# Optimization experiments

Hardware: AMD Instinct MI355X
Metric: run time of the kernel (lower is better)

The kernel has to match this reference:

```python
import jax, jax.numpy as jnp
import numpy as np

N_NODES = 50000
N_EDGES = 800000
D_IN = 128
D_HID = 128
D_OUT = 128
N_GRAPHS = 512


def _linear_params(key, d_in, d_out):
    kw, kb = jax.random.split(key)
    bound = 1.0 / np.sqrt(d_in)
    W = jax.random.uniform(kw, (d_in, d_out), minval=-bound, maxval=bound, dtype=jnp.float32)
    b = jax.random.uniform(kb, (d_out,), minval=-bound, maxval=bound, dtype=jnp.float32)
    return W, b


def setup_inputs() -> dict:
    key = jax.random.key(0)
    ks = jax.random.split(key, 8)
    x = jax.random.normal(ks[0], (N_NODES, D_IN), dtype=jnp.float32)
    edge_index = jax.random.randint(ks[1], (2, N_EDGES), 0, N_NODES, dtype=jnp.int64)
    batch = jnp.sort(jax.random.randint(ks[2], (N_NODES,), 0, N_GRAPHS, dtype=jnp.int64))
    W1a, b1a = _linear_params(ks[3], D_IN, D_HID)
    W1b, b1b = _linear_params(ks[4], D_HID, D_HID)
    W2a, b2a = _linear_params(ks[5], D_HID, D_HID)
    W2b, b2b = _linear_params(ks[6], D_HID, D_OUT)
    Wfc, bfc = _linear_params(ks[7], D_OUT, D_OUT)
    return {"x": x, "edge_index": edge_index, "batch": batch,
            "W1a": W1a, "b1a": b1a, "W1b": W1b, "b1b": b1b,
            "W2a": W2a, "b2a": b2a, "W2b": W2b, "b2b": b2b,
            "Wfc": Wfc, "bfc": bfc}


def _gin_conv(h, src, dst, Wa, ba, Wb, bb):
    # neighbor sum: gather source features, scatter-add to targets (eps=0)
    agg = jax.ops.segment_sum(h[src], dst, num_segments=N_NODES)
    z = h + agg  # (1+eps)*x + sum_neighbors, eps=0
    z = jax.nn.relu(z @ Wa + ba)
    return z @ Wb + bb


def reference(x, edge_index, batch, W1a, b1a, W1b, b1b, W2a, b2a, W2b, b2b, Wfc, bfc):
    src, dst = edge_index[0], edge_index[1]
    h = jax.nn.relu(_gin_conv(x, src, dst, W1a, b1a, W1b, b1b))
    h = jax.nn.relu(_gin_conv(h, src, dst, W2a, b2a, W2b, b2b))
    g = jax.ops.segment_sum(h, batch, num_segments=N_GRAPHS)  # global_add_pool
    return jax.nn.relu(g @ Wfc + bfc)
```

## Files before the change

### kernel.cpp

```cpp
#include <hip/hip_runtime.h>

#define N_NODES 50000
#define N_EDGES 800000
#define N_GRAPHS 512
#define CAP 48
#define ZN N_NODES

typedef __bf16 bf16x8 __attribute__((ext_vector_type(8)));
typedef float f32x4 __attribute__((ext_vector_type(4)));
typedef unsigned short u16;
typedef unsigned int u32;

__device__ __forceinline__ u16 f2bf(float f) {
    union { float f; u32 i; } v; v.f = f;
    u32 r = v.i + 0x7fffu + ((v.i >> 16) & 1u);
    return (u16)(r >> 16);
}
__device__ __forceinline__ float bf2f(u16 u) {
    union { u32 i; float f; } v; v.i = ((u32)u) << 16; return v.f;
}

__global__ void k_prep(const int* __restrict__ ei, int* __restrict__ cnt, u16* __restrict__ slots,
                       const float* __restrict__ X, u16* __restrict__ XB, u16* __restrict__ HB,
                       const float* __restrict__ W1a, const float* __restrict__ W1b,
                       const float* __restrict__ W2a, const float* __restrict__ W2b,
                       u16* __restrict__ T1a, u16* __restrict__ T1b,
                       u16* __restrict__ T2a, u16* __restrict__ T2b,
                       int E, int n4) {
    int bid = blockIdx.x;
    if (bid < 3125) {
        int e = bid * 256 + threadIdx.x;
        if (e < E) {
            int s = ei[e];
            int d = ei[E + e];
            int p = atomicAdd(&cnt[d * 4], 1);
            if (p < CAP) slots[(size_t)d * CAP + p] = (u16)s;
        }
    } else if (bid < 9375) {
        int i = (bid - 3125) * 256 + threadIdx.x;
        if (i < n4) {
            float4 v = ((const float4*)X)[i];
            ushort4 o;
            o.x = f2bf(v.x); o.y = f2bf(v.y); o.z = f2bf(v.z); o.w = f2bf(v.w);
            ((ushort4*)XB)[i] = o;
        }
    } else if (bid < 9631) {
        int b2 = bid - 9375;
        int widx = b2 >> 6;
        int i = (b2 & 63) * 256 + threadIdx.x;
        const float* W = widx == 0 ? W1a : widx == 1 ? W1b : widx == 2 ? W2a : W2b;
        u16* T = widx == 0 ? T1a : widx == 1 ? T1b : widx == 2 ? T2a : T2b;
        int k = i >> 7, n = i & 127;
        T[n * 128 + k] = f2bf(W[k * 128 + n]);
    } else {
        int t = threadIdx.x;
        if (t < 64)       ((u32*)XB)[(size_t)ZN * 64 + t]        = 0u;
        else if (t < 128) ((u32*)HB)[(size_t)ZN * 64 + (t - 64)] = 0u;
    }
}


#define STAGE16(BUF, CI, CJ)                                            \
    _Pragma("unroll")                                                   \
    for (int u = 0; u < 16; ++u) {                                      \
        u32 nb = (u32)smI[wv][(CI)][(CJ) + u];                          \
        BUF[u] = X2[(nb << 6) + lane];                                  \
    }

#define ACCUM16(BUF)                                                    \
    _Pragma("unroll")                                                   \
    for (int u = 0; u < 16; ++u) {                                      \
        ax += bf2f((u16)(BUF[u] & 0xffff));                             \
        ay += bf2f((u16)(BUF[u] >> 16));                                \
    }

#define FINROW(CI) {                                                    \
        int r = wv * 8 + (CI);                                          \
        smZu[(r * 16 + ((lane >> 2) ^ (r & 15))) * 4 + (lane & 3)] =    \
            (((u32)f2bf(ay)) << 16) | (u32)f2bf(ax);                    \
        ax = 0.f; ay = 0.f;                                             \
    }

#define AGG_PHASE()                                                                  \
    int degv = 0;                                                                    \
    {                                                                                \
        int gr = row0 + wv * 8 + lane;                                               \
        if (lane < 8 && gr < N) {                                                    \
            int d = cnt[gr * 4];                                                     \
            degv = d > CAP ? CAP : d;                                                \
        }                                                                            \
    }                                                                                \
    {                                                                                \
        u32 tv[8];                                                                   \
        int sl = lane - 1; sl = sl < 0 ? 0 : (sl >= CAP ? CAP - 1 : sl);             \
        _Pragma("unroll")                                                            \
        for (int i = 0; i < 8; ++i) {                                                \
            int gr = row0 + wv * 8 + i;                                              \
            tv[i] = (gr < N) ? (u32)slots[(size_t)gr * CAP + sl] : (u32)ZN;          \
        }                                                                            \
        _Pragma("unroll")                                                            \
        for (int i = 0; i < 8; ++i) {                                                \
            int gr = row0 + wv * 8 + i;                                              \
            int de = __builtin_amdgcn_readlane(degv, i) + 1;                         \
            u32 v = (lane == 0) ? (u32)gr : tv[i];                                   \
            if (gr >= N || lane >= de) v = ZN;                                       \
            smI[wv][i][lane] = (u16)v;                                               \
        }                                                                            \
    }                                                                                \
    {                                                                                \
        float ax = 0.f, ay = 0.f;                                                    \
        u32 bufA[16], bufB[16];                                                      \
        int ci = 0, cj = 0;                                                          \
        int de = __builtin_amdgcn_readlane(degv, 0) + 1;                             \
        STAGE16(bufA, 0, 0);                                                         \
        for (;;) {                                                                   \
            int ni = ci, nj = cj + 16;                                               \
            if (nj >= de) { ni = ci + 1; nj = 0; }                                   \
            int have = (ni < 8);                                                     \
            if (have) { de = __builtin_amdgcn_readlane(degv, ni) + 1;                \
                        STAGE16(bufB, ni, nj); }                                     \
            ACCUM16(bufA);                                                           \
            if (nj == 0) FINROW(ci);                                                 \
            if (!have) break;                                                        \
            ci = ni; cj = nj;                                                        \
            ni = ci; nj = cj + 16;                                                   \
            if (nj >= de) { ni = ci + 1; nj = 0; }                                   \
            have = (ni < 8);                                                         \
            if (have) { de = __builtin_amdgcn_readlane(degv, ni) + 1;                \
                        STAGE16(bufA, ni, nj); }                                     \
            ACCUM16(bufB);                                                           \
            if (nj == 0) FINROW(ci);                                                 \
            if (!have) break;                                                        \
            ci = ni; cj = nj;                                                        \
        }                                                                            \
    }

__global__ __launch_bounds__(512, 4)
void k_gin1(const u16* __restrict__ X, const int* __restrict__ cnt,
            const u16* __restrict__ slots,
            const u16* __restrict__ WaT, const float* __restrict__ ba,
            const u16* __restrict__ WbT, const float* __restrict__ bb,
            u16* __restrict__ H, int N) {
    __shared__ u16 smZ[64 * 128];
    __shared__ u16 smW[128 * 128];
    __shared__ u16 smI[8][8][64];
    uint4* smZ4 = (uint4*)smZ;
    uint4* smW4 = (uint4*)smW;
    u32* smZu = (u32*)smZ;

    const int tid = threadIdx.x;
    const int lane = tid & 63, wv = tid >> 6;
    const int q = lane >> 4, m = lane & 15;
    const int ws = wv & 3, wc = wv >> 2;
    const int row0 = blockIdx.x * 64;
    const u32* X2 = (const u32*)X;

    for (int i = tid; i < 2048; i += 512) {
        int r = i >> 4, c4 = i & 15;
        smW4[r * 16 + (c4 ^ (r & 15))] = ((const uint4*)WaT)[i];
    }

    AGG_PHASE();
    __syncthreads();

    f32x4 acc[4];
#pragma unroll
    for (int nt = 0; nt < 4; ++nt) acc[nt] = (f32x4){0.f, 0.f, 0.f, 0.f};
#pragma unroll
    for (int kt = 0; kt < 4; ++kt) {
        int r = ws * 16 + m;
        bf16x8 a = *(const bf16x8*)(smZ4 + (r * 16 + ((kt * 4 + q) ^ (r & 15))));
#pragma unroll
        for (int nt = 0; nt < 4; ++nt) {
            int n = (wc * 4 + nt) * 16 + m;
            bf16x8 bfr = *(const bf16x8*)(smW4 + (n * 16 + ((kt * 4 + q) ^ (n & 15))));
            acc[nt] = __builtin_amdgcn_mfma_f32_16x16x32_bf16(a, bfr, acc[nt], 0, 0, 0);
        }
    }
    __syncthreads();

    for (int i = tid; i < 2048; i += 512) {
        int r = i >> 4, c4 = i & 15;
        smW4[r * 16 + (c4 ^ (r & 15))] = ((const uint4*)WbT)[i];
    }
#pragma unroll
    for (int nt = 0; nt < 4; ++nt) {
        int col = (wc * 4 + nt) * 16 + m;
        float bias = ba[col];
        int c4 = col >> 3, ci8 = col & 7;
#pragma unroll
        for (int r2 = 0; r2 < 4; ++r2) {
            int row = ws * 16 + q * 4 + r2;
            float x = acc[nt][r2] + bias;
            x = x > 0.f ? x : 0.f;
            smZ[(row * 16 + (c4 ^ (row & 15))) * 8 + ci8] = f2bf(x);
        }
    }
    __syncthreads();

    f32x4 acc2[4];
#pragma unroll
    for (int nt = 0; nt < 4; ++nt) acc2[nt] = (f32x4){0.f, 0.f, 0.f, 0.f};
#pragma unroll
    for (int kt = 0; kt < 4; ++kt) {
        int r = ws * 16 + m;
        bf16x8 a = *(const bf16x8*)(smZ4 + (r * 16 + ((kt * 4 + q) ^ (r & 15))));
#pragma unroll
        for (int nt = 0; nt < 4; ++nt) {
            int n = (wc * 4 + nt) * 16 + m;
            bf16x8 bfr = *(const bf16x8*)(smW4 + (n * 16 + ((kt * 4 + q) ^ (n & 15))));
            acc2[nt] = __builtin_amdgcn_mfma_f32_16x16x32_bf16(a, bfr, acc2[nt], 0, 0, 0);
        }
    }
#pragma unroll
    for (int nt = 0; nt < 4; ++nt) {
        int col = (wc * 4 + nt) * 16 + m;
        float bias = bb[col];
#pragma unroll
        for (int r2 = 0; r2 < 4; ++r2) {
            int row = row0 + ws * 16 + q * 4 + r2;
            if (row < N) {
                float x = acc2[nt][r2] + bias;
                H[(size_t)row * 128 + col] = f2bf(x > 0.f ? x : 0.f);
            }
        }
    }
}

__global__ __launch_bounds__(512, 4)
void k_gin2(const u16* __restrict__ X, const int* __restrict__ cnt,
            const u16* __restrict__ slots,
            const u16* __restrict__ WaT, const float* __restrict__ ba,
            const u16* __restrict__ WbT, const float* __restrict__ bb,
            const int* __restrict__ batch, float* __restrict__ G, int N) {
    __shared__ u16 smZ[64 * 128];
    __shared__ u16 smW[128 * 128];
    __shared__ u16 smI[8][8][64];
    __shared__ int sb[64];
    uint4* smZ4 = (uint4*)smZ;
    uint4* smW4 = (uint4*)smW;
    u32* smZu = (u32*)smZ;

    const int tid = threadIdx.x;
    const int lane = tid & 63, wv = tid >> 6;
    const int q = lane >> 4, m = lane & 15;
    const int ws = wv & 3, wc = wv >> 2;
    const int row0 = blockIdx.x * 64;
    const u32* X2 = (const u32*)X;

    if (tid < 64) sb[tid] = (row0 + tid < N) ? batch[row0 + tid] : -1;

    for (int i = tid; i < 2048; i += 512) {
        int r = i >> 4, c4 = i & 15;
        smW4[r * 16 + (c4 ^ (r & 15))] = ((const uint4*)WaT)[i];
    }

    AGG_PHASE();
    __syncthreads();

    f32x4 acc[4];
#pragma unroll
    for (int nt = 0; nt < 4; ++nt) acc[nt] = (f32x4){0.f, 0.f, 0.f, 0.f};
#pragma unroll
    for (int kt = 0; kt < 4; ++kt) {
        int r = ws * 16 + m;
        bf16x8 a = *(const bf16x8*)(smZ4 + (r * 16 + ((kt * 4 + q) ^ (r & 15))));
#pragma unroll
        for (int nt = 0; nt < 4; ++nt) {
            int n = (wc * 4 + nt) * 16 + m;
            bf16x8 bfr = *(const bf16x8*)(smW4 + (n * 16 + ((kt * 4 + q) ^ (n & 15))));
            acc[nt] = __builtin_amdgcn_mfma_f32_16x16x32_bf16(a, bfr, acc[nt], 0, 0, 0);
        }
    }
    __syncthreads();

    for (int i = tid; i < 2048; i += 512) {
        int r = i >> 4, c4 = i & 15;
        smW4[r * 16 + (c4 ^ (r & 15))] = ((const uint4*)WbT)[i];
    }
#pragma unroll
    for (int nt = 0; nt < 4; ++nt) {
        int col = (wc * 4 + nt) * 16 + m;
        float bias = ba[col];
        int c4 = col >> 3, ci8 = col & 7;
#pragma unroll
        for (int r2 = 0; r2 < 4; ++r2) {
            int row = ws * 16 + q * 4 + r2;
            float x = acc[nt][r2] + bias;
            x = x > 0.f ? x : 0.f;
            smZ[(row * 16 + (c4 ^ (row & 15))) * 8 + ci8] = f2bf(x);
        }
    }
    __syncthreads();

    f32x4 acc2[4];
#pragma unroll
    for (int nt = 0; nt < 4; ++nt) acc2[nt] = (f32x4){0.f, 0.f, 0.f, 0.f};
#pragma unroll
    for (int kt = 0; kt < 4; ++kt) {
        int r = ws * 16 + m;
        bf16x8 a = *(const bf16x8*)(smZ4 + (r * 16 + ((kt * 4 + q) ^ (r & 15))));
#pragma unroll
        for (int nt = 0; nt < 4; ++nt) {
            int n = (wc * 4 + nt) * 16 + m;
            bf16x8 bfr = *(const bf16x8*)(smW4 + (n * 16 + ((kt * 4 + q) ^ (n & 15))));
            acc2[nt] = __builtin_amdgcn_mfma_f32_16x16x32_bf16(a, bfr, acc2[nt], 0, 0, 0);
        }
    }
#pragma unroll
    for (int nt = 0; nt < 4; ++nt) {
        int col = (wc * 4 + nt) * 16 + m;
        float bias = bb[col];
#pragma unroll
        for (int r2 = 0; r2 < 4; ++r2) {
            int row = ws * 16 + q * 4 + r2;
            float x = acc2[nt][r2] + bias;
            smZ[row * 128 + col] = f2bf(x > 0.f ? x : 0.f);
        }
    }
    __syncthreads();
    {
        int col = tid & 127, quarter = tid >> 7;
        int rbeg = quarter * 16, rend = rbeg + 16;
        float run = 0.f; int curg = -1;
        for (int r = rbeg; r < rend; ++r) {
            int gg = sb[r];
            if (gg < 0) break;
            if (gg != curg) {
                if (curg >= 0) atomicAdd(&G[curg * 128 + col], run);
                run = 0.f; curg = gg;
            }
            run += bf2f(smZ[r * 128 + col]);
        }
        if (curg >= 0) atomicAdd(&G[curg * 128 + col], run);
    }
}

__global__ void k_fc(const float* __restrict__ G, const float* __restrict__ W,
                     const float* __restrict__ bias, float* __restrict__ O) {
    __shared__ float gs[128];
    int t = threadIdx.x, gidx = blockIdx.x;
    gs[t] = G[gidx * 128 + t];
    __syncthreads();
    float acc = bias[t];
    for (int k = 0; k < 128; ++k)
        acc += gs[k] * W[k * 128 + t];
    acc = acc > 0.f ? acc : 0.f;
    O[gidx * 128 + t] = acc;
}

extern "C" void kernel_launch(void* const* d_in, const int* in_sizes, int n_in,
                              void* d_out, int out_size, void* d_ws, size_t ws_size,
                              hipStream_t stream) {
    const int N = N_NODES, E = N_EDGES, NG = N_GRAPHS;

    const float* x   = (const float*)d_in[0];
    const int* ei    = (const int*)d_in[1];
    const int* batch = (const int*)d_in[2];
    const float* W1a = (const float*)d_in[3];
    const float* b1a = (const float*)d_in[4];
    const float* W1b = (const float*)d_in[5];
    const float* b1b = (const float*)d_in[6];
    const float* W2a = (const float*)d_in[7];
    const float* b2a = (const float*)d_in[8];
    const float* W2b = (const float*)d_in[9];
    const float* b2b = (const float*)d_in[10];
    const float* Wfc = (const float*)d_in[11];
    const float* bfc = (const float*)d_in[12];
    float* out = (float*)d_out;

    char* w = (char*)d_ws;
    int* cnt    = (int*)(w + 0x0000000);
    float* g    = (float*)(w + 0x00C4000);
    u16* slots  = (u16*)(w + 0x0110000);
    u16* xb     = (u16*)(w + 0x05B0000);
    u16* hb     = (u16*)(w + 0x1F50000);
    u16* T1a    = (u16*)(w + 0x2C20000);
    u16* T1b    = (u16*)(w + 0x2C28000);
    u16* T2a    = (u16*)(w + 0x2C30000);
    u16* T2b    = (u16*)(w + 0x2C38000);

    (void)hipMemsetAsync(w, 0, 0x104000, stream);

    const int n4 = N * 128 / 4;
    k_prep<<<9632, 256, 0, stream>>>(ei, cnt, slots, x, xb, hb, W1a, W1b, W2a, W2b,
                                     T1a, T1b, T2a, T2b, E, n4);

    const int GINB = (N + 63) / 64;

    k_gin1<<<GINB, 512, 0, stream>>>(xb, cnt, slots, T1a, b1a, T1b, b1b, hb, N);
    k_gin2<<<GINB, 512, 0, stream>>>(hb, cnt, slots, T2a, b2a, T2b, b2b, batch, g, N);

    k_fc<<<NG, 128, 0, stream>>>(g, Wfc, bfc, out);
}
```

Baseline: 229.9 us.

## Bin edges per 64-node block and build neighbor lists in shared memory

Edge scatter now does one global atomic per 64-node destination block and appends packed (local dst, src) words into per-block bins, instead of one atomic per destination node into per-node slot arrays. Each GIN kernel reads its block's bin coalesced and builds per-row neighbor lists in LDS with shared atomics, with capacity raised to 64 per row. This is meant to cut contention and scattered global writes in the prep kernel and make the gather-index loads contiguous. In exchange it adds LDS atomics and an extra barrier inside both GIN kernels, and edges are dropped if a bin overflows its 1536 capacity.

```diff
diff --git a/kernel.cpp b/kernel.cpp
--- a/kernel.cpp
+++ b/kernel.cpp
@@ -3,8 +3,9 @@
 #define N_NODES 50000
 #define N_EDGES 800000
 #define N_GRAPHS 512
-#define CAP 48
 #define ZN N_NODES
+#define BCAP 1536
+#define RCAP 64
 
 typedef __bf16 bf16x8 __attribute__((ext_vector_type(8)));
 typedef float f32x4 __attribute__((ext_vector_type(4)));
@@ -20,7 +21,7 @@
     union { u32 i; float f; } v; v.i = ((u32)u) << 16; return v.f;
 }
 
-__global__ void k_prep(const int* __restrict__ ei, int* __restrict__ cnt, u16* __restrict__ slots,
+__global__ void k_prep(const int* __restrict__ ei, int* __restrict__ cur, u32* __restrict__ bins,
                        const float* __restrict__ X, u16* __restrict__ XB, u16* __restrict__ HB,
                        const float* __restrict__ W1a, const float* __restrict__ W1b,
                        const float* __restrict__ W2a, const float* __restrict__ W2b,
@@ -33,8 +34,9 @@
         if (e < E) {
             int s = ei[e];
             int d = ei[E + e];
-            int p = atomicAdd(&cnt[d * 4], 1);
-            if (p < CAP) slots[(size_t)d * CAP + p] = (u16)s;
+            int b = d >> 6;
+            int p = atomicAdd(&cur[b * 32], 1);
+            if (p < BCAP) bins[(size_t)b * BCAP + p] = (((u32)(d & 63)) << 16) | (u32)s;
         }
     } else if (bid < 9375) {
         int i = (bid - 3125) * 256 + threadIdx.x;
@@ -63,7 +65,7 @@
 #define STAGE16(BUF, CI, CJ)                                            \
     _Pragma("unroll")                                                   \
     for (int u = 0; u < 16; ++u) {                                      \
-        u32 nb = (u32)smI[wv][(CI)][(CJ) + u];                          \
+        u32 nb = (u32)smI[wv * 8 + (CI)][(CJ) + u];                     \
         BUF[u] = X2[(nb << 6) + lane];                                  \
     }
 
@@ -82,42 +84,46 @@
     }
 
 #define AGG_PHASE()                                                                  \
-    int degv = 0;                                                                    \
     {                                                                                \
-        int gr = row0 + wv * 8 + lane;                                               \
-        if (lane < 8 && gr < N) {                                                    \
-            int d = cnt[gr * 4];                                                     \
-            degv = d > CAP ? CAP : d;                                                \
+        const u32 fill = 0xC350C350u;                      \
+        int r = tid >> 3, c = tid & 7;                                               \
+        uint4 v4 = make_uint4(fill, fill, fill, fill);                               \
+        if (c == 0) {                                                                \
+            int gr = row0 + r;                                                       \
+            v4.x = (fill & 0xffff0000u) | (u32)((gr < N) ? gr : ZN);                 \
+        }                                                                            \
+        ((uint4*)smI)[tid] = v4;                                                     \
+        if (tid < 64) ldsCnt[tid] = 1;                                               \
+    }                                                                                \
+    __syncthreads();                                                                 \
+    {                                                                                \
+        int ecnt = cur[blockIdx.x * 32];                                             \
+        if (ecnt > BCAP) ecnt = BCAP;                                                \
+        const u32* myb = bins + (size_t)blockIdx.x * BCAP;                           \
+        for (int i = tid; i < ecnt; i += 512) {                                      \
+            u32 v = myb[i];                                                          \
+            int dl = v >> 16;                                                        \
+            int pos = atomicAdd(&ldsCnt[dl], 1);                                     \
+            if (pos < RCAP) smI[dl][pos] = (u16)(v & 0xffff);                        \
         }                                                                            \
     }                                                                                \
-    {                                                                                \
-        u32 tv[8];                                                                   \
-        int sl = lane - 1; sl = sl < 0 ? 0 : (sl >= CAP ? CAP - 1 : sl);             \
-        _Pragma("unroll")                                                            \
-        for (int i = 0; i < 8; ++i) {                                                \
-            int gr = row0 + wv * 8 + i;                                              \
-            tv[i] = (gr < N) ? (u32)slots[(size_t)gr * CAP + sl] : (u32)ZN;          \
-        }                                                                            \
-        _Pragma("unroll")                                                            \
-        for (int i = 0; i < 8; ++i) {                                                \
-            int gr = row0 + wv * 8 + i;                                              \
-            int de = __builtin_amdgcn_readlane(degv, i) + 1;                         \
-            u32 v = (lane == 0) ? (u32)gr : tv[i];                                   \
-            if (gr >= N || lane >= de) v = ZN;                                       \
-            smI[wv][i][lane] = (u16)v;                                               \
-        }                                                                            \
+    __syncthreads();                                                                 \
+    int degv = 0;                                                                    \
+    if (lane < 8) {                                                                  \
+        int d = ldsCnt[wv * 8 + lane];                                               \
+        degv = d > RCAP ? RCAP : d;                                                  \
     }                                                                                \
     {                                                                                \
         float ax = 0.f, ay = 0.f;                                                    \
         u32 bufA[16], bufB[16];                                                      \
         int ci = 0, cj = 0;                                                          \
-        int de = __builtin_amdgcn_readlane(degv, 0) + 1;                             \
+        int de = __builtin_amdgcn_readlane(degv, 0);                                 \
         STAGE16(bufA, 0, 0);                                                         \
         for (;;) {                                                                   \
             int ni = ci, nj = cj + 16;                                               \
             if (nj >= de) { ni = ci + 1; nj = 0; }                                   \
             int have = (ni < 8);                                                     \
-            if (have) { de = __builtin_amdgcn_readlane(degv, ni) + 1;                \
+            if (have) { de = __builtin_amdgcn_readlane(degv, ni);                    \
                         STAGE16(bufB, ni, nj); }                                     \
             ACCUM16(bufA);                                                           \
             if (nj == 0) FINROW(ci);                                                 \
@@ -126,7 +132,7 @@
             ni = ci; nj = cj + 16;                                                   \
             if (nj >= de) { ni = ci + 1; nj = 0; }                                   \
             have = (ni < 8);                                                         \
-            if (have) { de = __builtin_amdgcn_readlane(degv, ni) + 1;                \
+            if (have) { de = __builtin_amdgcn_readlane(degv, ni);                    \
                         STAGE16(bufA, ni, nj); }                                     \
             ACCUM16(bufB);                                                           \
             if (nj == 0) FINROW(ci);                                                 \
@@ -136,14 +142,15 @@
     }
 
 __global__ __launch_bounds__(512, 4)
-void k_gin1(const u16* __restrict__ X, const int* __restrict__ cnt,
-            const u16* __restrict__ slots,
+void k_gin1(const u16* __restrict__ X, const int* __restrict__ cur,
+            const u32* __restrict__ bins,
             const u16* __restrict__ WaT, const float* __restrict__ ba,
             const u16* __restrict__ WbT, const float* __restrict__ bb,
             u16* __restrict__ H, int N) {
     __shared__ u16 smZ[64 * 128];
     __shared__ u16 smW[128 * 128];
-    __shared__ u16 smI[8][8][64];
+    __shared__ u16 smI[64][RCAP];
+    __shared__ int ldsCnt[64];
     uint4* smZ4 = (uint4*)smZ;
     uint4* smW4 = (uint4*)smW;
     u32* smZu = (u32*)smZ;
@@ -228,14 +235,15 @@
 }
 
 __global__ __launch_bounds__(512, 4)
-void k_gin2(const u16* __restrict__ X, const int* __restrict__ cnt,
-            const u16* __restrict__ slots,
+void k_gin2(const u16* __restrict__ X, const int* __restrict__ cur,
+            const u32* __restrict__ bins,
             const u16* __restrict__ WaT, const float* __restrict__ ba,
             const u16* __restrict__ WbT, const float* __restrict__ bb,
             const int* __restrict__ batch, float* __restrict__ G, int N) {
     __shared__ u16 smZ[64 * 128];
     __shared__ u16 smW[128 * 128];
-    __shared__ u16 smI[8][8][64];
+    __shared__ u16 smI[64][RCAP];
+    __shared__ int ldsCnt[64];
     __shared__ int sb[64];
     uint4* smZ4 = (uint4*)smZ;
     uint4* smW4 = (uint4*)smW;
@@ -248,7 +256,10 @@
     const int row0 = blockIdx.x * 64;
     const u32* X2 = (const u32*)X;
 
-    if (tid < 64) sb[tid] = (row0 + tid < N) ? batch[row0 + tid] : -1;
+    if (tid >= 448 && tid < 512) {
+        int t = tid - 448;
+        sb[t] = (row0 + t < N) ? batch[row0 + t] : -1;
+    }
 
     for (int i = tid; i < 2048; i += 512) {
         int r = i >> 4, c4 = i & 15;
@@ -370,26 +381,26 @@
     float* out = (float*)d_out;
 
     char* w = (char*)d_ws;
-    int* cnt    = (int*)(w + 0x0000000);
-    float* g    = (float*)(w + 0x00C4000);
-    u16* slots  = (u16*)(w + 0x0110000);
-    u16* xb     = (u16*)(w + 0x05B0000);
-    u16* hb     = (u16*)(w + 0x1F50000);
-    u16* T1a    = (u16*)(w + 0x2C20000);
-    u16* T1b    = (u16*)(w + 0x2C28000);
-    u16* T2a    = (u16*)(w + 0x2C30000);
-    u16* T2b    = (u16*)(w + 0x2C38000);
-
-    (void)hipMemsetAsync(w, 0, 0x104000, stream);
+    int* cur    = (int*)(w + 0x0000000);
+    float* g    = (float*)(w + 0x0019000);
+    u32* bins   = (u32*)(w + 0x0060000);
+    u16* xb     = (u16*)(w + 0x0500000);
+    u16* hb     = (u16*)(w + 0x1200000);
+    u16* T1a    = (u16*)(w + 0x1F00000);
+    u16* T1b    = (u16*)(w + 0x1F08000);
+    u16* T2a    = (u16*)(w + 0x1F10000);
+    u16* T2b    = (u16*)(w + 0x1F18000);
+
+    (void)hipMemsetAsync(w, 0, 0x59000, stream);
 
     const int n4 = N * 128 / 4;
-    k_prep<<<9632, 256, 0, stream>>>(ei, cnt, slots, x, xb, hb, W1a, W1b, W2a, W2b,
+    k_prep<<<9632, 256, 0, stream>>>(ei, cur, bins, x, xb, hb, W1a, W1b, W2a, W2b,
                                      T1a, T1b, T2a, T2b, E, n4);
 
     const int GINB = (N + 63) / 64;
 
-    k_gin1<<<GINB, 512, 0, stream>>>(xb, cnt, slots, T1a, b1a, T1b, b1b, hb, N);
-    k_gin2<<<GINB, 512, 0, stream>>>(hb, cnt, slots, T2a, b2a, T2b, b2b, batch, g, N);
+    k_gin1<<<GINB, 512, 0, stream>>>(xb, cur, bins, T1a, b1a, T1b, b1b, hb, N);
+    k_gin2<<<GINB, 512, 0, stream>>>(hb, cur, bins, T2a, b2a, T2b, b2b, batch, g, N);
 
     k_fc<<<NG, 128, 0, stream>>>(g, Wfc, bfc, out);
 }
```

Result: no change. 232.4 us (+1.1%).
